# Optimization experiments

Measured on AMD Instinct MI355X. Metric: run time of the kernel, lower is better.

## Reference

```python
import jax, jax.numpy as jnp
import numpy as np

B, T, D = 4, 1024, 1024   # batch, block_size, d_model
H, HS = 16, 64            # n_head, head_size


def setup_inputs() -> dict:
    key = jax.random.key(0)
    ks = jax.random.split(key, 6)
    s = 0.02  # small init like nn.Linear default scale
    return {
        "x": jax.random.normal(ks[0], (B, T, D), jnp.float32),
        "Wq": jax.random.normal(ks[1], (H, D, HS), jnp.float32) * s,
        "Wk": jax.random.normal(ks[2], (H, D, HS), jnp.float32) * s,
        "Wv": jax.random.normal(ks[3], (H, D, HS), jnp.float32) * s,
        "Wo": jax.random.normal(ks[4], (H * HS, D), jnp.float32) * s,
        "bo": jnp.zeros((D,), jnp.float32),
    }


def reference(x, Wq, Wk, Wv, Wo, bo):
    # Batched equivalent of the per-head loop: all heads in one einsum.
    q = jnp.einsum('btd,hde->bhte', x, Wq)   # [B,H,T,HS]
    k = jnp.einsum('btd,hde->bhte', x, Wk)
    v = jnp.einsum('btd,hde->bhte', x, Wv)
    scores = jnp.einsum('bhte,bhse->bhts', q, k) * (HS ** -0.5)  # [B,H,T,T]
    causal = jnp.tril(jnp.ones((T, T), dtype=bool))
    scores = jnp.where(causal, scores, -jnp.inf)
    att = jax.nn.softmax(scores, axis=-1)
    out = jnp.einsum('bhts,bhse->bhte', att, v)                  # [B,H,T,HS]
    out = out.transpose(0, 2, 1, 3).reshape(B, T, H * HS)        # concat heads
    return out @ Wo + bo                                         # proj to d_model
```

## Files before the change

### kernel.cpp

```cpp
#include <hip/hip_runtime.h>
#include <math.h>

#define NB 4
#define SEQ 1024
#define DM 1024
#define NH 16
#define HS 64

typedef __attribute__((ext_vector_type(8))) short short8;
typedef __attribute__((ext_vector_type(4))) short short4v;
typedef __attribute__((ext_vector_type(4))) float floatx4;

#define MFMA(a, b, c) __builtin_amdgcn_mfma_f32_16x16x32_bf16((a), (b), (c), 0, 0, 0)

static __device__ __forceinline__ unsigned short f2bf(float f) {
  unsigned int u = __float_as_uint(f);
  u += 0x7FFFu + ((u >> 16) & 1u);
  return (unsigned short)(u >> 16);
}

static __device__ __forceinline__ void g2l(const unsigned short* g, short* l) {
  __builtin_amdgcn_global_load_lds(
      (const __attribute__((address_space(1))) void*)g,
      (__attribute__((address_space(3))) void*)l, 16, 0, 0);
}

#define SWZ_SRC(tid) ((((tid) & 7) ^ (((tid) >> 3) & 7)) << 3)
#define SWZ_RD(B, r) ((((B) ^ ((r) & 7)) << 3))

__global__ __launch_bounds__(256) void prep_all(
    const float* __restrict__ x,
    const float* __restrict__ Wq, const float* __restrict__ Wk,
    const float* __restrict__ Wv, const float* __restrict__ Wo,
    unsigned short* __restrict__ xb,
    unsigned short* __restrict__ Wtq, unsigned short* __restrict__ Wtk,
    unsigned short* __restrict__ Wtv, unsigned short* __restrict__ Wot) {
  __shared__ __align__(16) short Ts[64 * 72];
  const int tid = threadIdx.x;
  const int mat = blockIdx.y;
  if (mat == 4) {
    int base = blockIdx.x * 4096;
#pragma unroll
    for (int i = 0; i < 16; i++) {
      int idx4 = base + tid + i * 256;
      float4 v = *(const float4*)(x + (size_t)idx4 * 4);
      short4v o;
      o[0] = (short)f2bf(v.x); o[1] = (short)f2bf(v.y);
      o[2] = (short)f2bf(v.z); o[3] = (short)f2bf(v.w);
      *(short4v*)(xb + (size_t)idx4 * 4) = o;
    }
    return;
  }
  const float* src;
  unsigned short* dst;
  int r0, c0;
  if (mat < 3) {
    src = (mat == 0) ? Wq : (mat == 1) ? Wk : Wv;
    dst = (mat == 0) ? Wtq : (mat == 1) ? Wtk : Wtv;
    int h = blockIdx.x >> 4;
    int d0 = (blockIdx.x & 15) * 64;
    src += (size_t)(h * DM + d0) * HS;
    dst += (size_t)(h * HS) * DM + d0;
    r0 = HS;  c0 = DM;
  } else {
    src = Wo; dst = Wot;
    int k0 = (blockIdx.x >> 4) * 64;
    int n0 = (blockIdx.x & 15) * 64;
    src += (size_t)k0 * DM + n0;
    dst += (size_t)n0 * DM + k0;
    r0 = DM;  c0 = DM;
  }
#pragma unroll
  for (int i = 0; i < 4; i++) {
    int p = tid + i * 256;
    int row = p >> 4, c4 = (p & 15) << 2;
    float4 v = *(const float4*)(src + (size_t)row * r0 + c4);
    Ts[(c4 + 0) * 72 + row] = (short)f2bf(v.x);
    Ts[(c4 + 1) * 72 + row] = (short)f2bf(v.y);
    Ts[(c4 + 2) * 72 + row] = (short)f2bf(v.z);
    Ts[(c4 + 3) * 72 + row] = (short)f2bf(v.w);
  }
  __syncthreads();
#pragma unroll
  for (int i = 0; i < 2; i++) {
    int p = tid + i * 256;
    int row = p >> 3, c8 = (p & 7) << 3;
    *(short8*)(dst + (size_t)row * c0 + c8) = *(const short8*)&Ts[row * 72 + c8];
  }
}

__global__ __launch_bounds__(256, 3) void qkv_gemm128(
    const unsigned short* __restrict__ xb,
    const unsigned short* __restrict__ Wcat,
    unsigned short* __restrict__ qo,
    unsigned short* __restrict__ ko,
    unsigned short* __restrict__ vo) {
  __shared__ __align__(16) short As[128 * 64];
  __shared__ __align__(16) short Bs[128 * 64];
  const int tid = threadIdx.x;
  const int bm = blockIdx.x, bn = blockIdx.y;
  const int lane = tid & 63, wave = tid >> 6;
  const int quad = lane >> 4, l16 = lane & 15;
  const int wr = wave >> 1, wc = wave & 1;
  const int l7 = l16 & 7;
  const floatx4 fzero = {0.f, 0.f, 0.f, 0.f};

  floatx4 acc[4][4];
#pragma unroll
  for (int i = 0; i < 4; i++)
#pragma unroll
    for (int j = 0; j < 4; j++) acc[i][j] = fzero;

  const int srow = tid >> 3;
  const int scolw = SWZ_SRC(tid);
  const unsigned short* Ag = xb + (size_t)(bm * 128 + srow) * DM + scolw;
  const unsigned short* Bg = Wcat + (size_t)(bn * 128 + srow) * DM + scolw;
  short* Ad = As + tid * 8;
  short* Bd = Bs + tid * 8;

  for (int k0 = 0; k0 < DM; k0 += 64) {
    __syncthreads();
#pragma unroll
    for (int i = 0; i < 4; i++) g2l(Ag + (size_t)i * 32 * DM + k0, Ad + i * 2048);
#pragma unroll
    for (int i = 0; i < 4; i++) g2l(Bg + (size_t)i * 32 * DM + k0, Bd + i * 2048);
    __syncthreads();

    short8 af[4][2], bf[4][2];
#pragma unroll
    for (int ti = 0; ti < 4; ti++)
#pragma unroll
      for (int kh = 0; kh < 2; kh++)
        af[ti][kh] = *(const short8*)&As[(wr * 64 + ti * 16 + l16) * 64 +
                                          SWZ_RD(kh * 4 + quad, l7)];
#pragma unroll
    for (int tj = 0; tj < 4; tj++)
#pragma unroll
      for (int kh = 0; kh < 2; kh++)
        bf[tj][kh] = *(const short8*)&Bs[(wc * 64 + tj * 16 + l16) * 64 +
                                          SWZ_RD(kh * 4 + quad, l7)];
#pragma unroll
    for (int ti = 0; ti < 4; ti++)
#pragma unroll
      for (int tj = 0; tj < 4; tj++) {
        acc[ti][tj] = MFMA(af[ti][0], bf[tj][0], acc[ti][tj]);
        acc[ti][tj] = MFMA(af[ti][1], bf[tj][1], acc[ti][tj]);
      }
  }

  const int mat = bn >> 3;
  const int mbase = bm * 128 + wr * 64 + quad * 4;
  const int nn0 = (bn & 7) * 128 + wc * 64;
  if (mat < 2) {
    unsigned short* dst = (mat == 0) ? qo : ko;
#pragma unroll
    for (int ti = 0; ti < 4; ti++)
#pragma unroll
      for (int tj = 0; tj < 4; tj++) {
        int ecol = nn0 + tj * 16 + l16;
        int h = ecol >> 6, e = ecol & 63;
#pragma unroll
        for (int r = 0; r < 4; r++) {
          int m = mbase + ti * 16 + r;
          int b = m >> 10, t = m & (SEQ - 1);
          dst[((size_t)(b * NH + h) * SEQ + t) * HS + e] = f2bf(acc[ti][tj][r]);
        }
      }
  } else {
#pragma unroll
    for (int ti = 0; ti < 4; ti++)
#pragma unroll
      for (int tj = 0; tj < 4; tj++) {
        int ecol = nn0 + tj * 16 + l16;
        int h = ecol >> 6, e = ecol & 63;
        int m0 = mbase + ti * 16;
        int b = m0 >> 10, t0 = m0 & (SEQ - 1);
        short4v pv;
#pragma unroll
        for (int r = 0; r < 4; r++) pv[r] = (short)f2bf(acc[ti][tj][r]);
        *(short4v*)&vo[((size_t)(b * NH + h) * HS + e) * SEQ + t0] = pv;
      }
  }
}

__global__ __launch_bounds__(512) void attn_kernel(
    const unsigned short* __restrict__ q,
    const unsigned short* __restrict__ k,
    const unsigned short* __restrict__ v,
    unsigned short* __restrict__ o)
{
  __shared__ __align__(16) short Qs[128 * 64];
  __shared__ __align__(16) short Ks[2][64 * 64];
  __shared__ __align__(16) short Vt[2][64 * 64];
  __shared__ __align__(16) short Ps[128 * 76];
  const int tid = threadIdx.x;
  const int lid = (int)blockIdx.x;
  const int jj = lid & 3, half = lid >> 8, pp = (lid >> 2) & 63;
  const int qt = half ? jj : 7 - jj;
  const int h = pp & 15, b = pp >> 4;
  const int lane = tid & 63, wave = tid >> 6;
  const int quad = lane >> 4, l16 = lane & 15;
  const int l7 = l16 & 7;
  const size_t bh = (size_t)(b * NH + h) * SEQ * HS;
  const unsigned short* qp = q + bh + (size_t)qt * 128 * HS;
  const unsigned short* kbase = k + bh;
  const unsigned short* vbase = v + (size_t)(b * NH + h) * HS * SEQ;
  const floatx4 fzero = {0.f, 0.f, 0.f, 0.f};
  const float c2 = 0.125f * 1.44269504089f;
  const float C0 = 16.0f * 1.44269504089f;
  const int srow = tid >> 3;
  const int scolw = SWZ_SRC(tid);

#pragma unroll
  for (int i = 0; i < 2; i++)
    g2l(qp + (size_t)(srow + i * 64) * HS + scolw, Qs + tid * 8 + i * 4096);
  g2l(kbase + (size_t)srow * HS + scolw, &Ks[0][tid * 8]);
  g2l(vbase + (size_t)srow * SEQ + scolw, &Vt[0][tid * 8]);
  __syncthreads();

  short8 qa[2];
#pragma unroll
  for (int kh = 0; kh < 2; kh++)
    qa[kh] = *(const short8*)&Qs[(wave * 16 + l16) * 64 +
                                  SWZ_RD(kh * 4 + quad, l7)];

  const int rowbase = qt * 128 + wave * 16;
  float l_[4];
  floatx4 O[4];
#pragma unroll
  for (int r = 0; r < 4; r++) l_[r] = 0.f;
#pragma unroll
  for (int tj = 0; tj < 4; tj++) O[tj] = fzero;

  const int ktmax = 2 * qt + 1;
  for (int kt = 0; kt <= ktmax; kt++) {
    const int cur = kt & 1;
    if (kt < ktmax) {
      g2l(kbase + (size_t)(kt + 1) * 64 * HS + (size_t)srow * HS + scolw,
          &Ks[1 - cur][tid * 8]);
      g2l(vbase + (size_t)srow * SEQ + (kt + 1) * 64 + scolw,
          &Vt[1 - cur][tid * 8]);
    }

    if (kt * 64 <= rowbase + 15) {
      floatx4 S[4];
#pragma unroll
      for (int tj = 0; tj < 4; tj++) {
        short8 b0 = *(const short8*)&Ks[cur][(tj * 16 + l16) * 64 + SWZ_RD(quad, l7)];
        short8 b1 = *(const short8*)&Ks[cur][(tj * 16 + l16) * 64 + SWZ_RD(4 + quad, l7)];
        floatx4 s = fzero;
        s = MFMA(qa[0], b0, s);
        s = MFMA(qa[1], b1, s);
        S[tj] = s;
      }
      if (kt * 64 + 63 > rowbase) {
#pragma unroll
        for (int tj = 0; tj < 4; tj++) {
          int col = kt * 64 + tj * 16 + l16;
#pragma unroll
          for (int r = 0; r < 4; r++) {
            int row = rowbase + quad * 4 + r;
            if (col > row) S[tj][r] = -INFINITY;
          }
        }
      }
#pragma unroll
      for (int tj = 0; tj < 4; tj++)
#pragma unroll
        for (int r = 0; r < 4; r++) {
          float pv = __builtin_amdgcn_exp2f(S[tj][r] * c2 - C0);
          S[tj][r] = pv;
          l_[r] += pv;
        }
#pragma unroll
      for (int tj = 0; tj < 4; tj++)
#pragma unroll
        for (int r = 0; r < 4; r++)
          Ps[(wave * 16 + quad * 4 + r) * 76 + tj * 16 + l16] =
              (short)f2bf(S[tj][r]);

      short8 pa[2];
#pragma unroll
      for (int kh = 0; kh < 2; kh++)
        pa[kh] = *(const short8*)&Ps[(wave * 16 + l16) * 76 + kh * 32 + quad * 8];
#pragma unroll
      for (int tj = 0; tj < 4; tj++) {
        short8 b0 = *(const short8*)&Vt[cur][(tj * 16 + l16) * 64 + SWZ_RD(quad, l7)];
        short8 b1 = *(const short8*)&Vt[cur][(tj * 16 + l16) * 64 + SWZ_RD(4 + quad, l7)];
        O[tj] = MFMA(pa[0], b0, O[tj]);
        O[tj] = MFMA(pa[1], b1, O[tj]);
      }
    }
    __syncthreads();
  }

#pragma unroll
  for (int r = 0; r < 4; r++) {
    float lsum = l_[r];
#pragma unroll
    for (int off = 1; off < 16; off <<= 1)
      lsum += __shfl_xor(lsum, off, 16);
    float inv = 1.0f / lsum;
    int t = qt * 128 + wave * 16 + quad * 4 + r;
#pragma unroll
    for (int tj = 0; tj < 4; tj++) {
      int e = tj * 16 + l16;
      o[((size_t)(b * SEQ + t)) * DM + h * HS + e] = f2bf(O[tj][r] * inv);
    }
  }
}

__global__ __launch_bounds__(256, 3) void out_gemm64(
    const unsigned short* __restrict__ A,
    const unsigned short* __restrict__ Bt,
    const float* __restrict__ bo,
    float* __restrict__ out) {
  __shared__ __align__(16) short As[128 * 64];
  __shared__ __align__(16) short Bs[64 * 64];
  const int tid = threadIdx.x;
  const int bm = blockIdx.x, bn = blockIdx.y;
  const int lane = tid & 63, wave = tid >> 6;
  const int quad = lane >> 4, l16 = lane & 15;
  const int wr = wave >> 1, wc = wave & 1;
  const int l7 = l16 & 7;
  const floatx4 fzero = {0.f, 0.f, 0.f, 0.f};

  floatx4 acc[4][2];
#pragma unroll
  for (int i = 0; i < 4; i++)
#pragma unroll
    for (int j = 0; j < 2; j++) acc[i][j] = fzero;

  const int srow = tid >> 3;
  const int scolw = SWZ_SRC(tid);
  const unsigned short* Ag = A + (size_t)(bm * 128 + srow) * DM + scolw;
  const unsigned short* Bg = Bt + (size_t)(bn * 64 + srow) * DM + scolw;
  short* Ad = As + tid * 8;
  short* Bd = Bs + tid * 8;

  for (int k0 = 0; k0 < DM; k0 += 64) {
    __syncthreads();
#pragma unroll
    for (int i = 0; i < 4; i++) g2l(Ag + (size_t)i * 32 * DM + k0, Ad + i * 2048);
#pragma unroll
    for (int i = 0; i < 2; i++) g2l(Bg + (size_t)i * 32 * DM + k0, Bd + i * 2048);
    __syncthreads();

    short8 af[4][2], bf[2][2];
#pragma unroll
    for (int ti = 0; ti < 4; ti++)
#pragma unroll
      for (int kh = 0; kh < 2; kh++)
        af[ti][kh] = *(const short8*)&As[(wr * 64 + ti * 16 + l16) * 64 +
                                          SWZ_RD(kh * 4 + quad, l7)];
#pragma unroll
    for (int tj = 0; tj < 2; tj++)
#pragma unroll
      for (int kh = 0; kh < 2; kh++)
        bf[tj][kh] = *(const short8*)&Bs[(wc * 32 + tj * 16 + l16) * 64 +
                                          SWZ_RD(kh * 4 + quad, l7)];
#pragma unroll
    for (int ti = 0; ti < 4; ti++)
#pragma unroll
      for (int tj = 0; tj < 2; tj++) {
        acc[ti][tj] = MFMA(af[ti][0], bf[tj][0], acc[ti][tj]);
        acc[ti][tj] = MFMA(af[ti][1], bf[tj][1], acc[ti][tj]);
      }
  }

#pragma unroll
  for (int ti = 0; ti < 4; ti++)
#pragma unroll
    for (int tj = 0; tj < 2; tj++) {
      int n = bn * 64 + wc * 32 + tj * 16 + l16;
      float bias = bo[n];
#pragma unroll
      for (int r = 0; r < 4; r++) {
        int m = bm * 128 + wr * 64 + ti * 16 + quad * 4 + r;
        out[(size_t)m * DM + n] = acc[ti][tj][r] + bias;
      }
    }
}

extern "C" void kernel_launch(void* const* d_in, const int* in_sizes, int n_in,
                              void* d_out, int out_size, void* d_ws, size_t ws_size,
                              hipStream_t stream) {
  const float* x  = (const float*)d_in[0];
  const float* Wq = (const float*)d_in[1];
  const float* Wk = (const float*)d_in[2];
  const float* Wv = (const float*)d_in[3];
  const float* Wo = (const float*)d_in[4];
  const float* bo = (const float*)d_in[5];
  float* out = (float*)d_out;

  const size_t nx = (size_t)NB * SEQ * DM;
  const size_t nw = (size_t)DM * DM;
  unsigned short* xb  = (unsigned short*)d_ws;
  unsigned short* wtq = xb + nx;
  unsigned short* wtk = wtq + nw;
  unsigned short* wtv = wtk + nw;
  unsigned short* wot = wtv + nw;
  unsigned short* qws = wot + nw;
  unsigned short* kws = qws + nx;
  unsigned short* vws = kws + nx;
  unsigned short* aws = vws + nx;

  prep_all<<<dim3(256, 5), dim3(256), 0, stream>>>(x, Wq, Wk, Wv, Wo,
                                                   xb, wtq, wtk, wtv, wot);
  qkv_gemm128<<<dim3(32, 24), dim3(256), 0, stream>>>(xb, wtq, qws, kws, vws);
  attn_kernel<<<dim3(512), dim3(512), 0, stream>>>(qws, kws, vws, aws);
  out_gemm64<<<dim3(32, 16), dim3(256), 0, stream>>>(aws, wot, bo, out);
}
```

Before: 155.5 us.

## Shrink attention query tile to 64 rows, single-buffer K/V, reorder blocks

The attention kernel now uses 64-row query tiles with 256-thread blocks (1024 blocks) instead of 128-row tiles with 512 threads. K/V double-buffering is dropped in favour of a single buffer loaded between two barriers, which cuts LDS use so more blocks can be resident. Block-to-tile mapping is changed to a four-group interleave meant to balance causal work. The cost is exposed K/V load latency on every iteration and extra K/V reloads per query row.

```diff
diff --git a/kernel.cpp b/kernel.cpp
--- a/kernel.cpp
+++ b/kernel.cpp
@@ -183,26 +183,27 @@
   }
 }
 
-__global__ __launch_bounds__(512) void attn_kernel(
+__global__ __launch_bounds__(256) void attn_kernel(
     const unsigned short* __restrict__ q,
     const unsigned short* __restrict__ k,
     const unsigned short* __restrict__ v,
     unsigned short* __restrict__ o)
 {
-  __shared__ __align__(16) short Qs[128 * 64];
-  __shared__ __align__(16) short Ks[2][64 * 64];
-  __shared__ __align__(16) short Vt[2][64 * 64];
-  __shared__ __align__(16) short Ps[128 * 76];
+  __shared__ __align__(16) short Qs[64 * 64];
+  __shared__ __align__(16) short Ks[64 * 64];
+  __shared__ __align__(16) short Vt[64 * 64];
+  __shared__ __align__(16) short Ps[64 * 76];
   const int tid = threadIdx.x;
   const int lid = (int)blockIdx.x;
-  const int jj = lid & 3, half = lid >> 8, pp = (lid >> 2) & 63;
-  const int qt = half ? jj : 7 - jj;
-  const int h = pp & 15, b = pp >> 4;
+  const int g = lid >> 8, cc = lid & 255;
+  const int j = cc >> 6, bhid = cc & 63;
+  const int qt = (g == 0) ? j : (g == 1) ? 15 - j : (g == 2) ? 7 - j : 8 + j;
+  const int h = bhid & 15, b = bhid >> 4;
   const int lane = tid & 63, wave = tid >> 6;
   const int quad = lane >> 4, l16 = lane & 15;
   const int l7 = l16 & 7;
   const size_t bh = (size_t)(b * NH + h) * SEQ * HS;
-  const unsigned short* qp = q + bh + (size_t)qt * 128 * HS;
+  const unsigned short* qp = q + bh + (size_t)qt * 64 * HS;
   const unsigned short* kbase = k + bh;
   const unsigned short* vbase = v + (size_t)(b * NH + h) * HS * SEQ;
   const floatx4 fzero = {0.f, 0.f, 0.f, 0.f};
@@ -212,10 +213,11 @@
   const int scolw = SWZ_SRC(tid);
 
 #pragma unroll
-  for (int i = 0; i < 2; i++)
-    g2l(qp + (size_t)(srow + i * 64) * HS + scolw, Qs + tid * 8 + i * 4096);
-  g2l(kbase + (size_t)srow * HS + scolw, &Ks[0][tid * 8]);
-  g2l(vbase + (size_t)srow * SEQ + scolw, &Vt[0][tid * 8]);
+  for (int i = 0; i < 2; i++) {
+    g2l(qp + (size_t)(srow + i * 32) * HS + scolw, Qs + tid * 8 + i * 2048);
+    g2l(kbase + (size_t)(srow + i * 32) * HS + scolw, Ks + tid * 8 + i * 2048);
+    g2l(vbase + (size_t)(srow + i * 32) * SEQ + scolw, Vt + tid * 8 + i * 2048);
+  }
   __syncthreads();
 
   short8 qa[2];
@@ -224,7 +226,7 @@
     qa[kh] = *(const short8*)&Qs[(wave * 16 + l16) * 64 +
                                   SWZ_RD(kh * 4 + quad, l7)];
 
-  const int rowbase = qt * 128 + wave * 16;
+  const int rowbase = qt * 64 + wave * 16;
   float l_[4];
   floatx4 O[4];
 #pragma unroll
@@ -232,66 +234,66 @@
 #pragma unroll
   for (int tj = 0; tj < 4; tj++) O[tj] = fzero;
 
-  const int ktmax = 2 * qt + 1;
-  for (int kt = 0; kt <= ktmax; kt++) {
-    const int cur = kt & 1;
-    if (kt < ktmax) {
-      g2l(kbase + (size_t)(kt + 1) * 64 * HS + (size_t)srow * HS + scolw,
-          &Ks[1 - cur][tid * 8]);
-      g2l(vbase + (size_t)srow * SEQ + (kt + 1) * 64 + scolw,
-          &Vt[1 - cur][tid * 8]);
-    }
-
-    if (kt * 64 <= rowbase + 15) {
-      floatx4 S[4];
+  for (int kt = 0; kt <= qt; kt++) {
+    floatx4 S[4];
+#pragma unroll
+    for (int tj = 0; tj < 4; tj++) {
+      short8 b0 = *(const short8*)&Ks[(tj * 16 + l16) * 64 + SWZ_RD(quad, l7)];
+      short8 b1 = *(const short8*)&Ks[(tj * 16 + l16) * 64 + SWZ_RD(4 + quad, l7)];
+      floatx4 s = fzero;
+      s = MFMA(qa[0], b0, s);
+      s = MFMA(qa[1], b1, s);
+      S[tj] = s;
+    }
+    if (kt == qt) {
 #pragma unroll
       for (int tj = 0; tj < 4; tj++) {
-        short8 b0 = *(const short8*)&Ks[cur][(tj * 16 + l16) * 64 + SWZ_RD(quad, l7)];
-        short8 b1 = *(const short8*)&Ks[cur][(tj * 16 + l16) * 64 + SWZ_RD(4 + quad, l7)];
-        floatx4 s = fzero;
-        s = MFMA(qa[0], b0, s);
-        s = MFMA(qa[1], b1, s);
-        S[tj] = s;
-      }
-      if (kt * 64 + 63 > rowbase) {
-#pragma unroll
-        for (int tj = 0; tj < 4; tj++) {
-          int col = kt * 64 + tj * 16 + l16;
-#pragma unroll
-          for (int r = 0; r < 4; r++) {
-            int row = rowbase + quad * 4 + r;
-            if (col > row) S[tj][r] = -INFINITY;
-          }
+        int col = kt * 64 + tj * 16 + l16;
+#pragma unroll
+        for (int r = 0; r < 4; r++) {
+          int row = rowbase + quad * 4 + r;
+          if (col > row) S[tj][r] = -INFINITY;
         }
       }
-#pragma unroll
-      for (int tj = 0; tj < 4; tj++)
-#pragma unroll
-        for (int r = 0; r < 4; r++) {
-          float pv = __builtin_amdgcn_exp2f(S[tj][r] * c2 - C0);
-          S[tj][r] = pv;
-          l_[r] += pv;
-        }
-#pragma unroll
-      for (int tj = 0; tj < 4; tj++)
-#pragma unroll
-        for (int r = 0; r < 4; r++)
-          Ps[(wave * 16 + quad * 4 + r) * 76 + tj * 16 + l16] =
-              (short)f2bf(S[tj][r]);
-
-      short8 pa[2];
-#pragma unroll
-      for (int kh = 0; kh < 2; kh++)
-        pa[kh] = *(const short8*)&Ps[(wave * 16 + l16) * 76 + kh * 32 + quad * 8];
-#pragma unroll
-      for (int tj = 0; tj < 4; tj++) {
-        short8 b0 = *(const short8*)&Vt[cur][(tj * 16 + l16) * 64 + SWZ_RD(quad, l7)];
-        short8 b1 = *(const short8*)&Vt[cur][(tj * 16 + l16) * 64 + SWZ_RD(4 + quad, l7)];
-        O[tj] = MFMA(pa[0], b0, O[tj]);
-        O[tj] = MFMA(pa[1], b1, O[tj]);
-      }
-    }
-    __syncthreads();
+    }
+#pragma unroll
+    for (int tj = 0; tj < 4; tj++)
+#pragma unroll
+      for (int r = 0; r < 4; r++) {
+        float pv = __builtin_amdgcn_exp2f(S[tj][r] * c2 - C0);
+        S[tj][r] = pv;
+        l_[r] += pv;
+      }
+#pragma unroll
+    for (int tj = 0; tj < 4; tj++)
+#pragma unroll
+      for (int r = 0; r < 4; r++)
+        Ps[(wave * 16 + quad * 4 + r) * 76 + tj * 16 + l16] =
+            (short)f2bf(S[tj][r]);
+
+    short8 pa[2];
+#pragma unroll
+    for (int kh = 0; kh < 2; kh++)
+      pa[kh] = *(const short8*)&Ps[(wave * 16 + l16) * 76 + kh * 32 + quad * 8];
+#pragma unroll
+    for (int tj = 0; tj < 4; tj++) {
+      short8 b0 = *(const short8*)&Vt[(tj * 16 + l16) * 64 + SWZ_RD(quad, l7)];
+      short8 b1 = *(const short8*)&Vt[(tj * 16 + l16) * 64 + SWZ_RD(4 + quad, l7)];
+      O[tj] = MFMA(pa[0], b0, O[tj]);
+      O[tj] = MFMA(pa[1], b1, O[tj]);
+    }
+
+    if (kt < qt) {
+      __syncthreads();
+#pragma unroll
+      for (int i = 0; i < 2; i++) {
+        g2l(kbase + (size_t)(kt + 1) * 64 * HS + (size_t)(srow + i * 32) * HS + scolw,
+            Ks + tid * 8 + i * 2048);
+        g2l(vbase + (size_t)(srow + i * 32) * SEQ + (kt + 1) * 64 + scolw,
+            Vt + tid * 8 + i * 2048);
+      }
+      __syncthreads();
+    }
   }
 
 #pragma unroll
@@ -301,7 +303,7 @@
     for (int off = 1; off < 16; off <<= 1)
       lsum += __shfl_xor(lsum, off, 16);
     float inv = 1.0f / lsum;
-    int t = qt * 128 + wave * 16 + quad * 4 + r;
+    int t = qt * 64 + wave * 16 + quad * 4 + r;
 #pragma unroll
     for (int tj = 0; tj < 4; tj++) {
       int e = tj * 16 + l16;
@@ -408,6 +410,6 @@
   prep_all<<<dim3(256, 5), dim3(256), 0, stream>>>(x, Wq, Wk, Wv, Wo,
                                                    xb, wtq, wtk, wtv, wot);
   qkv_gemm128<<<dim3(32, 24), dim3(256), 0, stream>>>(xb, wtq, qws, kws, vws);
-  attn_kernel<<<dim3(512), dim3(512), 0, stream>>>(qws, kws, vws, aws);
+  attn_kernel<<<dim3(1024), dim3(256), 0, stream>>>(qws, kws, vws, aws);
   out_gemm64<<<dim3(32, 16), dim3(256), 0, stream>>>(aws, wot, bo, out);
 }
```

Result: no change. 153.6 us (-1.2%).
